# Performance work log

Measured on AMD Instinct MI355X. Metric: run time of the kernel, lower is better.

Reference implementation:

```python
import jax, jax.numpy as jnp
import numpy as np

N_NODES = 50000
N_EDGES = 500000
HIDDEN = 128
HEADS = 8
HEAD_DIM = HIDDEN // HEADS


def setup_inputs() -> dict:
    key = jax.random.key(0)
    ks = jax.random.split(key, 20)

    def lin_w(k, fin, fout):
        return (jax.random.normal(k, (fin, fout), jnp.float32) / np.sqrt(fin)).astype(jnp.float32)

    inp = {
        "h": jax.random.normal(ks[0], (N_NODES, HIDDEN), jnp.float32),
        "x": jax.random.normal(ks[1], (N_NODES, 3), jnp.float32),
        "src": jax.random.randint(ks[2], (N_EDGES,), 0, N_NODES, jnp.int32),
        "dst": jax.random.randint(ks[3], (N_EDGES,), 0, N_NODES, jnp.int32),
        "distances": jax.random.uniform(ks[4], (N_EDGES,), jnp.float32),
        # linear layers stored as [in, out] (transposed vs torch nn.Linear)
        "Wq": lin_w(ks[5], HIDDEN, HIDDEN), "bq": jnp.zeros((HIDDEN,), jnp.float32),
        "Wk": lin_w(ks[6], HIDDEN, HIDDEN), "bk": jnp.zeros((HIDDEN,), jnp.float32),
        "Wv": lin_w(ks[7], HIDDEN, HIDDEN), "bv": jnp.zeros((HIDDEN,), jnp.float32),
        "Wo": lin_w(ks[8], HIDDEN, HIDDEN), "bo": jnp.zeros((HIDDEN,), jnp.float32),
        "Wd": lin_w(ks[9], 1, HEADS), "bd": jnp.zeros((HEADS,), jnp.float32),
        "Wg1": lin_w(ks[10], HIDDEN, HIDDEN), "bg1": jnp.zeros((HIDDEN,), jnp.float32),
        "Wg2": lin_w(ks[11], HIDDEN, 1), "bg2": jnp.zeros((1,), jnp.float32),
    }
    return inp


def reference(h, x, src, dst, distances,
              Wq, bq, Wk, bk, Wv, bv, Wo, bo, Wd, bd, Wg1, bg1, Wg2, bg2):
    n = h.shape[0]
    heads = Wd.shape[1]
    dh = Wq.shape[1] // heads

    q = (h @ Wq + bq).reshape(n, heads, dh)
    k = (h @ Wk + bk).reshape(n, heads, dh)
    v = (h @ Wv + bv).reshape(n, heads, dh)

    q_src = q[src]            # [E, heads, dh]
    k_dst = k[dst]
    v_dst = v[dst]

    logits = jnp.einsum('ehd,ehd->eh', q_src, k_dst) / jnp.sqrt(jnp.asarray(dh, h.dtype))
    bias = (distances * distances)[:, None] @ Wd + bd      # [E, heads]
    lg = logits - bias

    # segment softmax over edges grouped by src node
    m = jax.ops.segment_max(lg, src, num_segments=n)        # [N, heads]
    ex = jnp.exp(lg - m[src])
    s = jax.ops.segment_sum(ex, src, num_segments=n)
    w = ex / jnp.maximum(s[src], 1e-9)                      # [E, heads]

    h_upd = jax.ops.segment_sum(v_dst * w[:, :, None], src, num_segments=n)
    h_out = h + h_upd.reshape(n, heads * dh) @ Wo + bo

    w_mean = w.mean(axis=1)                                 # mean over heads -> [E]
    disp = jax.ops.segment_sum((x[dst] - x[src]) * w_mean[:, None], src, num_segments=n)

    gate = jnp.tanh(jax.nn.silu(h_out @ Wg1 + bg1) @ Wg2 + bg2)  # [N, 1]
    x_out = x + gate * disp
    return (h_out, x_out)
```

## Files before the change

### kernel.cpp

```cpp
#include <hip/hip_runtime.h>
#include <math.h>

#define N_NODES 50000
#define N_EDGES 500000
#define HIDDEN 128
#define HEADS 8
#define HEAD_DIM 16

#define QKV_BLOCKS 1563
#define SCAT_BLOCKS 1954
#define SPLITW_BLOCKS 320
#define ZERO_BLOCKS 196

typedef __attribute__((ext_vector_type(8))) short short8;
typedef __attribute__((ext_vector_type(4))) float floatx4;

#define OFF_Q       0u
#define OFF_KV      6400000u
#define OFF_HHI     12800000u
#define OFF_HLO     16000000u
#define OFF_DISP    19200000u
#define OFF_CNT     19350016u
#define OFF_ROWPTR  19400032u
#define OFF_CURSOR  19450048u
#define OFF_ESD     19500064u
#define OFF_WSPLIT  20500064u

static __device__ __forceinline__ unsigned short f2bf(float f) {
    unsigned u = __builtin_bit_cast(unsigned, f);
    unsigned r = (u + 0x7FFFu + ((u >> 16) & 1u)) >> 16;
    return (unsigned short)r;
}
static __device__ __forceinline__ float bf2f(unsigned short s) {
    return __builtin_bit_cast(float, (unsigned)s << 16);
}

__global__ void k_prep(const float* __restrict__ Wq, const float* __restrict__ Wk,
                       const float* __restrict__ Wv, const float* __restrict__ Wo,
                       const float* __restrict__ Wg1, unsigned short* __restrict__ ws,
                       int* __restrict__ cnt) {
    if (blockIdx.x >= SPLITW_BLOCKS) {
        int i = (blockIdx.x - SPLITW_BLOCKS) * 256 + threadIdx.x;
        if (i < N_NODES) cnt[i] = 0;
        return;
    }
    int t = blockIdx.x * 256 + threadIdx.x;
    int m = t >> 14, r = t & 16383;
    int k = r >> 7, n = r & 127;
    const float* W = (m == 0) ? Wq : (m == 1) ? Wk : (m == 2) ? Wv : (m == 3) ? Wo : Wg1;
    float x = W[k * 128 + n];
    int kc = k >> 5, kin = k & 31, quad = kin >> 3, j = kin & 7;
    int ct = n >> 4, nin = n & 15, lane = quad * 16 + nin;
    unsigned base = ((((unsigned)(m * 4 + kc) * 8 + ct) * 2) * 64 + lane) * 8 + j;
    unsigned short a = f2bf(x);
    ws[base] = a;
    ws[base + 512] = f2bf(x - bf2f(a));
}

__global__ void k_count(const int* __restrict__ src, int* __restrict__ cnt) {
    int e = blockIdx.x * 256 + threadIdx.x;
    if (e < N_EDGES) atomicAdd(&cnt[src[e]], 1);
}

__global__ __launch_bounds__(1024) void k_scan1(const int* __restrict__ cnt,
                                                int* __restrict__ loc,
                                                int* __restrict__ bsum, int n) {
    __shared__ int buf[1024];
    int t = threadIdx.x;
    int i = blockIdx.x * 1024 + t;
    int val = (i < n) ? cnt[i] : 0;
    buf[t] = val;
    __syncthreads();
    for (int off = 1; off < 1024; off <<= 1) {
        int a = (t >= off) ? buf[t - off] : 0;
        __syncthreads();
        buf[t] += a;
        __syncthreads();
    }
    if (i < n) loc[i] = buf[t];
    if (t == 1023) bsum[blockIdx.x] = buf[1023];
}

__global__ __launch_bounds__(256) void k_scan23(const int* __restrict__ cnt,
                                                const int* __restrict__ loc,
                                                const int* __restrict__ bsum,
                                                int* __restrict__ rowptr,
                                                int* __restrict__ cursor, int n, int nb) {
    __shared__ int sb[64];
    int t = threadIdx.x;
    if (t < 64) {
        int v = (t < nb) ? bsum[t] : 0;
        for (int off = 1; off < 64; off <<= 1) {
            int a = __shfl_up(v, off);
            if (t >= off) v += a;
        }
        sb[t] = v;
    }
    __syncthreads();
    int i = blockIdx.x * 256 + t;
    if (i < n) {
        int off = (i >= 1024) ? sb[(i >> 10) - 1] : 0;
        int incl = loc[i] + off;
        rowptr[i + 1] = incl;
        cursor[i] = incl - cnt[i];
    }
    if (i == 0) rowptr[0] = 0;
}

__global__ __launch_bounds__(256) void k_qkv_scatter(
    const float* __restrict__ h, const unsigned short* __restrict__ wsp,
    const float* __restrict__ bq, const float* __restrict__ bk, const float* __restrict__ bv,
    float* __restrict__ q, unsigned* __restrict__ kvp,
    const int* __restrict__ src, const int* __restrict__ dst,
    const float* __restrict__ dist, int* __restrict__ cursor, int2* __restrict__ esd) {
    if (blockIdx.x >= QKV_BLOCKS) {
        int e = (blockIdx.x - QKV_BLOCKS) * 256 + threadIdx.x;
        if (e < N_EDGES) {
            int pos = atomicAdd(&cursor[src[e]], 1);
            float dd = dist[e];
            esd[pos] = make_int2(dst[e], __float_as_int(dd * dd));
        }
        return;
    }

    const int wave = threadIdx.x >> 6, lane = threadIdx.x & 63;
    const int quad = lane >> 4, l15 = lane & 15;
    const int ct0 = wave * 2;
    const int row0 = blockIdx.x * 32;

    floatx4 acc[3][2][2];
#pragma unroll
    for (int m = 0; m < 3; ++m)
#pragma unroll
        for (int c = 0; c < 2; ++c)
#pragma unroll
            for (int r = 0; r < 2; ++r) acc[m][c][r] = (floatx4){0.f, 0.f, 0.f, 0.f};

#pragma unroll
    for (int kc = 0; kc < 4; ++kc) {
        short8 ah[2], al[2];
#pragma unroll
        for (int rt = 0; rt < 2; ++rt) {
            int row = row0 + rt * 16 + l15;
            if (row >= N_NODES) row = N_NODES - 1;
            const float* hp = h + (size_t)row * 128 + kc * 32 + quad * 8;
            float4 f0 = *(const float4*)(hp);
            float4 f1 = *(const float4*)(hp + 4);
            float fv[8] = {f0.x, f0.y, f0.z, f0.w, f1.x, f1.y, f1.z, f1.w};
#pragma unroll
            for (int j = 0; j < 8; ++j) {
                unsigned short hi = f2bf(fv[j]);
                ah[rt][j] = (short)hi;
                al[rt][j] = (short)f2bf(fv[j] - bf2f(hi));
            }
        }
#pragma unroll
        for (int m = 0; m < 3; ++m) {
#pragma unroll
            for (int ctl = 0; ctl < 2; ++ctl) {
                unsigned fb = ((((unsigned)(m * 4 + kc) * 8 + (ct0 + ctl)) * 2) * 64 + lane) * 8;
                short8 bh = *(const short8*)(wsp + fb);
                short8 bl = *(const short8*)(wsp + fb + 512);
#pragma unroll
                for (int rt = 0; rt < 2; ++rt) {
                    acc[m][ctl][rt] = __builtin_amdgcn_mfma_f32_16x16x32_bf16(
                        ah[rt], bh, acc[m][ctl][rt], 0, 0, 0);
                    acc[m][ctl][rt] = __builtin_amdgcn_mfma_f32_16x16x32_bf16(
                        ah[rt], bl, acc[m][ctl][rt], 0, 0, 0);
                    acc[m][ctl][rt] = __builtin_amdgcn_mfma_f32_16x16x32_bf16(
                        al[rt], bh, acc[m][ctl][rt], 0, 0, 0);
                }
            }
        }
    }

#pragma unroll
    for (int ctl = 0; ctl < 2; ++ctl) {
        int col = (ct0 + ctl) * 16 + l15;
        float bq_ = bq[col], bk_ = bk[col], bv_ = bv[col];
#pragma unroll
        for (int rt = 0; rt < 2; ++rt) {
#pragma unroll
            for (int reg = 0; reg < 4; ++reg) {
                int row = row0 + rt * 16 + quad * 4 + reg;
                if (row < N_NODES) {
                    q[(size_t)row * 128 + col] = acc[0][ctl][rt][reg] + bq_;
                    unsigned kb = f2bf(acc[1][ctl][rt][reg] + bk_);
                    unsigned vb = f2bf(acc[2][ctl][rt][reg] + bv_);
                    kvp[(size_t)row * 128 + col] = kb | (vb << 16);
                }
            }
        }
    }
}

__global__ __launch_bounds__(256) void k_edge_node(
    const float* __restrict__ q, const unsigned* __restrict__ kvp,
    const float* __restrict__ x,
    const int2* __restrict__ esd, const int* __restrict__ rowptr,
    const float* __restrict__ Wd, const float* __restrict__ bd,
    unsigned short* __restrict__ hupd_hi, unsigned short* __restrict__ hupd_lo,
    float* __restrict__ disp) {
    const int wave = threadIdx.x >> 6, lane = threadIdx.x & 63;
    const int node = blockIdx.x * 4 + wave;
    const int h = lane >> 3, sub = lane & 7;
    const int beg = rowptr[node], end = rowptr[node + 1];

    const float2 qv = *(const float2*)(q + (size_t)node * 128 + 2 * lane);
    const float wdh = Wd[h], bdh = bd[h];
    const bool dal = (sub < 3);
    float xs = dal ? x[node * 3 + sub] : 0.f;
    const unsigned colo = 2 * lane;

    float acc0 = 0.f, acc1 = 0.f, s_own = 0.f, da = 0.f;

    for (int cb = beg; cb < end; cb += 64) {
        int idx = cb + lane;
        int dvec = 0; float d2vec = 0.f;
        if (idx < end) {
            int2 ed = esd[idx];
            dvec = ed.x;
            d2vec = __int_as_float(ed.y);
        }
        int clen = min(64, end - cb);
        int i = 0;
        for (; i + 4 <= clen; i += 4) {
            int di[4]; float dd2[4]; uint2 kv2[4]; float xg[4];
#pragma unroll
            for (int j = 0; j < 4; ++j) {
                di[j]  = __shfl(dvec, i + j);
                dd2[j] = __shfl(d2vec, i + j);
            }
#pragma unroll
            for (int j = 0; j < 4; ++j)
                kv2[j] = *(const uint2*)(kvp + (unsigned)di[j] * 128u + colo);
#pragma unroll
            for (int j = 0; j < 4; ++j)
                xg[j] = dal ? x[(unsigned)di[j] * 3u + sub] : 0.f;
#pragma unroll
            for (int j = 0; j < 4; ++j) {
                float k0 = __builtin_bit_cast(float, kv2[j].x << 16);
                float v0 = __builtin_bit_cast(float, kv2[j].x & 0xFFFF0000u);
                float k1 = __builtin_bit_cast(float, kv2[j].y << 16);
                float v1 = __builtin_bit_cast(float, kv2[j].y & 0xFFFF0000u);
                float p = qv.x * k0 + qv.y * k1;
                p += __shfl_xor(p, 1);
                p += __shfl_xor(p, 2);
                p += __shfl_xor(p, 4);
                float w = __expf(p * 0.25f - (dd2[j] * wdh + bdh));
                s_own += w;
                acc0 += v0 * w;
                acc1 += v1 * w;
                da += (xg[j] - xs) * w;
            }
        }
        for (; i < clen; ++i) {
            int dij  = __shfl(dvec, i);
            float d2 = __shfl(d2vec, i);
            uint2 kv2 = *(const uint2*)(kvp + (unsigned)dij * 128u + colo);
            float xgj = dal ? x[(unsigned)dij * 3u + sub] : 0.f;
            float k0 = __builtin_bit_cast(float, kv2.x << 16);
            float v0 = __builtin_bit_cast(float, kv2.x & 0xFFFF0000u);
            float k1 = __builtin_bit_cast(float, kv2.y << 16);
            float v1 = __builtin_bit_cast(float, kv2.y & 0xFFFF0000u);
            float p = qv.x * k0 + qv.y * k1;
            p += __shfl_xor(p, 1);
            p += __shfl_xor(p, 2);
            p += __shfl_xor(p, 4);
            float w = __expf(p * 0.25f - (d2 * wdh + bdh));
            s_own += w;
            acc0 += v0 * w;
            acc1 += v1 * w;
            da += (xgj - xs) * w;
        }
    }

    float inva = 1.f / fmaxf(s_own, 1e-9f);
    float o0 = acc0 * inva, o1 = acc1 * inva;
    unsigned short h0 = f2bf(o0), h1 = f2bf(o1);
    unsigned short l0 = f2bf(o0 - bf2f(h0)), l1 = f2bf(o1 - bf2f(h1));
    ((unsigned*)hupd_hi)[(size_t)node * 64 + lane] = (unsigned)h0 | ((unsigned)h1 << 16);
    ((unsigned*)hupd_lo)[(size_t)node * 64 + lane] = (unsigned)l0 | ((unsigned)l1 << 16);

    da *= 0.125f * inva;
    da += __shfl_xor(da, 8);
    da += __shfl_xor(da, 16);
    da += __shfl_xor(da, 32);
    if (lane < 3) disp[node * 3 + lane] = da;
}

__global__ __launch_bounds__(256) void k_hout_gate(
    const float* __restrict__ h,
    const unsigned short* __restrict__ hupd_hi, const unsigned short* __restrict__ hupd_lo,
    const unsigned short* __restrict__ wsp,
    const float* __restrict__ bo, const float* __restrict__ bg1,
    const float* __restrict__ Wg2, const float* __restrict__ bg2,
    const float* __restrict__ x, const float* __restrict__ disp,
    float* __restrict__ hout, float* __restrict__ xout) {
    __shared__ float hb[4][16 * 132];
    const int wave = threadIdx.x >> 6, lane = threadIdx.x & 63;
    const int quad = lane >> 4, l15 = lane & 15;
    const int row0 = blockIdx.x * 64 + wave * 16;
    float* hbw = hb[wave];

    floatx4 acc[8];
#pragma unroll
    for (int c = 0; c < 8; ++c) acc[c] = (floatx4){0.f, 0.f, 0.f, 0.f};
#pragma unroll
    for (int kc = 0; kc < 4; ++kc) {
        int row = row0 + l15;
        if (row >= N_NODES) row = N_NODES - 1;
        size_t aoff = (size_t)row * 128 + kc * 32 + quad * 8;
        short8 ah = *(const short8*)(hupd_hi + aoff);
        short8 al = *(const short8*)(hupd_lo + aoff);
#pragma unroll
        for (int ct = 0; ct < 8; ++ct) {
            unsigned fb = ((((unsigned)(3 * 4 + kc) * 8 + ct) * 2) * 64 + lane) * 8;
            short8 bh = *(const short8*)(wsp + fb);
            short8 bl = *(const short8*)(wsp + fb + 512);
            acc[ct] = __builtin_amdgcn_mfma_f32_16x16x32_bf16(ah, bh, acc[ct], 0, 0, 0);
            acc[ct] = __builtin_amdgcn_mfma_f32_16x16x32_bf16(ah, bl, acc[ct], 0, 0, 0);
            acc[ct] = __builtin_amdgcn_mfma_f32_16x16x32_bf16(al, bh, acc[ct], 0, 0, 0);
        }
    }

#pragma unroll
    for (int ct = 0; ct < 8; ++ct) {
        int col = ct * 16 + l15;
        float bias = bo[col];
#pragma unroll
        for (int reg = 0; reg < 4; ++reg) {
            int row = row0 + quad * 4 + reg;
            float val = acc[ct][reg] + bias;
            if (row < N_NODES) {
                val += h[(size_t)row * 128 + col];
                hout[(size_t)row * 128 + col] = val;
            }
            hbw[(quad * 4 + reg) * 132 + col] = val;
        }
    }
    __asm__ volatile("s_waitcnt lgkmcnt(0)" ::: "memory");

    floatx4 acc2[8];
#pragma unroll
    for (int c = 0; c < 8; ++c) acc2[c] = (floatx4){0.f, 0.f, 0.f, 0.f};
#pragma unroll
    for (int kc = 0; kc < 4; ++kc) {
        const float* ap = hbw + l15 * 132 + kc * 32 + quad * 8;
        float4 f0 = *(const float4*)(ap);
        float4 f1 = *(const float4*)(ap + 4);
        float fv[8] = {f0.x, f0.y, f0.z, f0.w, f1.x, f1.y, f1.z, f1.w};
        short8 ah, al;
#pragma unroll
        for (int j = 0; j < 8; ++j) {
            unsigned short hi = f2bf(fv[j]);
            ah[j] = (short)hi;
            al[j] = (short)f2bf(fv[j] - bf2f(hi));
        }
#pragma unroll
        for (int ct = 0; ct < 8; ++ct) {
            unsigned fb = ((((unsigned)(4 * 4 + kc) * 8 + ct) * 2) * 64 + lane) * 8;
            short8 bh = *(const short8*)(wsp + fb);
            short8 bl = *(const short8*)(wsp + fb + 512);
            acc2[ct] = __builtin_amdgcn_mfma_f32_16x16x32_bf16(ah, bh, acc2[ct], 0, 0, 0);
            acc2[ct] = __builtin_amdgcn_mfma_f32_16x16x32_bf16(ah, bl, acc2[ct], 0, 0, 0);
            acc2[ct] = __builtin_amdgcn_mfma_f32_16x16x32_bf16(al, bh, acc2[ct], 0, 0, 0);
        }
    }

    float pr[4] = {0.f, 0.f, 0.f, 0.f};
#pragma unroll
    for (int ct = 0; ct < 8; ++ct) {
        int col = ct * 16 + l15;
        float b1 = bg1[col];
        float w2 = Wg2[col];
#pragma unroll
        for (int reg = 0; reg < 4; ++reg) {
            float z = acc2[ct][reg] + b1;
            pr[reg] += (z / (1.f + __expf(-z))) * w2;
        }
    }
#pragma unroll
    for (int off = 1; off < 16; off <<= 1) {
#pragma unroll
        for (int reg = 0; reg < 4; ++reg) pr[reg] += __shfl_xor(pr[reg], off);
    }
    if (l15 == 0) {
        float b2 = bg2[0];
#pragma unroll
        for (int reg = 0; reg < 4; ++reg) {
            int row = row0 + quad * 4 + reg;
            if (row < N_NODES) {
                float g = tanhf(pr[reg] + b2);
#pragma unroll
                for (int dd = 0; dd < 3; ++dd) {
                    int oo = row * 3 + dd;
                    xout[oo] = x[oo] + g * disp[oo];
                }
            }
        }
    }
}

extern "C" void kernel_launch(void* const* d_in, const int* in_sizes, int n_in,
                              void* d_out, int out_size, void* d_ws, size_t ws_size,
                              hipStream_t stream) {
    const float* h    = (const float*)d_in[0];
    const float* x    = (const float*)d_in[1];
    const int*   src  = (const int*)d_in[2];
    const int*   dst  = (const int*)d_in[3];
    const float* dist = (const float*)d_in[4];
    const float* Wq = (const float*)d_in[5];  const float* bq = (const float*)d_in[6];
    const float* Wk = (const float*)d_in[7];  const float* bk = (const float*)d_in[8];
    const float* Wv = (const float*)d_in[9];  const float* bv = (const float*)d_in[10];
    const float* Wo = (const float*)d_in[11]; const float* bo = (const float*)d_in[12];
    const float* Wd = (const float*)d_in[13]; const float* bd = (const float*)d_in[14];
    const float* Wg1 = (const float*)d_in[15]; const float* bg1 = (const float*)d_in[16];
    const float* Wg2 = (const float*)d_in[17]; const float* bg2 = (const float*)d_in[18];

    float* ws    = (float*)d_ws;
    float* q     = ws + OFF_Q;
    unsigned* kvp = (unsigned*)(ws + OFF_KV);
    float* disp  = ws + OFF_DISP;
    int* cnt     = (int*)(ws + OFF_CNT);
    int* rowptr  = (int*)(ws + OFF_ROWPTR);
    int* cursor  = (int*)(ws + OFF_CURSOR);
    int2* esd    = (int2*)(ws + OFF_ESD);
    unsigned short* wsp = (unsigned short*)(ws + OFF_WSPLIT);
    int* loc    = (int*)(ws + OFF_Q);
    int* bsum   = (int*)(ws + OFF_Q + 500000u);
    unsigned short* hupd_hi = (unsigned short*)(ws + OFF_HHI);
    unsigned short* hupd_lo = (unsigned short*)(ws + OFF_HLO);
    float* hout = (float*)d_out;
    float* xout = hout + (size_t)N_NODES * HIDDEN;

    const int nscan = (N_NODES + 1023) / 1024;

    k_prep<<<SPLITW_BLOCKS + ZERO_BLOCKS, 256, 0, stream>>>(Wq, Wk, Wv, Wo, Wg1, wsp, cnt);
    k_count<<<SCAT_BLOCKS, 256, 0, stream>>>(src, cnt);
    k_scan1<<<nscan, 1024, 0, stream>>>(cnt, loc, bsum, N_NODES);
    k_scan23<<<ZERO_BLOCKS, 256, 0, stream>>>(cnt, loc, bsum, rowptr, cursor, N_NODES, nscan);
    k_qkv_scatter<<<QKV_BLOCKS + SCAT_BLOCKS, 256, 0, stream>>>(
        h, wsp, bq, bk, bv, q, kvp, src, dst, dist, cursor, esd);
    k_edge_node<<<N_NODES / 4, 256, 0, stream>>>(q, kvp, x, esd, rowptr,
                                                 Wd, bd, hupd_hi, hupd_lo, disp);
    k_hout_gate<<<(N_NODES + 63) / 64, 256, 0, stream>>>(h, hupd_hi, hupd_lo, wsp,
                                                         bo, bg1, Wg2, bg2,
                                                         x, disp, hout, xout);
}
```

Baseline: 269.5 us.

## Stage QKV weight splits in LDS and precompute edge ranks to drop scatter atomics

The QKV projection now gives each block 128 rows. It splits the work into Q blocks and fused K/V blocks, and each of those stages a 64KB hi/lo bf16 weight matrix into LDS, where every wave reuses it across all 8 column tiles. Before, each wave read its weight fragments straight from global memory. The edge scatter also changes: the count kernel records each edge's rank within its source node, so the scatter computes positions from rowptr plus rank instead of doing a second atomic on a cursor array. The costs are a large LDS footprint, which limits occupancy, and an extra rank array stored in the h_upd scratch region. There are also fewer, heavier blocks, and the K/V blocks run two serial stage phases.

After: 259.8 us. 3.6% less time.

```diff
diff --git a/kernel.cpp b/kernel.cpp
--- a/kernel.cpp
+++ b/kernel.cpp
@@ -7,7 +7,8 @@
 #define HEADS 8
 #define HEAD_DIM 16
 
-#define QKV_BLOCKS 1563
+#define QB 391
+#define QKV_TOTAL 782
 #define SCAT_BLOCKS 1954
 #define SPLITW_BLOCKS 320
 #define ZERO_BLOCKS 196
@@ -40,7 +41,7 @@
                        const float* __restrict__ Wg1, unsigned short* __restrict__ ws,
                        int* __restrict__ cnt) {
     if (blockIdx.x >= SPLITW_BLOCKS) {
-        int i = (blockIdx.x - SPLITW_BLOCKS) * 256 + threadIdx.x;
+        int i = (int)(blockIdx.x - SPLITW_BLOCKS) * 256 + threadIdx.x;
         if (i < N_NODES) cnt[i] = 0;
         return;
     }
@@ -57,9 +58,10 @@
     ws[base + 512] = f2bf(x - bf2f(a));
 }
 
-__global__ void k_count(const int* __restrict__ src, int* __restrict__ cnt) {
+__global__ void k_count(const int* __restrict__ src, int* __restrict__ cnt,
+                        int* __restrict__ rnk) {
     int e = blockIdx.x * 256 + threadIdx.x;
-    if (e < N_EDGES) atomicAdd(&cnt[src[e]], 1);
+    if (e < N_EDGES) rnk[e] = atomicAdd(&cnt[src[e]], 1);
 }
 
 __global__ __launch_bounds__(1024) void k_scan1(const int* __restrict__ cnt,
@@ -81,11 +83,9 @@
     if (t == 1023) bsum[blockIdx.x] = buf[1023];
 }
 
-__global__ __launch_bounds__(256) void k_scan23(const int* __restrict__ cnt,
-                                                const int* __restrict__ loc,
+__global__ __launch_bounds__(256) void k_scan23(const int* __restrict__ loc,
                                                 const int* __restrict__ bsum,
-                                                int* __restrict__ rowptr,
-                                                int* __restrict__ cursor, int n, int nb) {
+                                                int* __restrict__ rowptr, int n, int nb) {
     __shared__ int sb[64];
     int t = threadIdx.x;
     if (t < 64) {
@@ -100,96 +100,149 @@
     int i = blockIdx.x * 256 + t;
     if (i < n) {
         int off = (i >= 1024) ? sb[(i >> 10) - 1] : 0;
-        int incl = loc[i] + off;
-        rowptr[i + 1] = incl;
-        cursor[i] = incl - cnt[i];
+        rowptr[i + 1] = loc[i] + off;
     }
     if (i == 0) rowptr[0] = 0;
 }
 
-__global__ __launch_bounds__(256) void k_qkv_scatter(
+__global__ __launch_bounds__(256, 2) void k_qkv_scatter(
     const float* __restrict__ h, const unsigned short* __restrict__ wsp,
     const float* __restrict__ bq, const float* __restrict__ bk, const float* __restrict__ bv,
     float* __restrict__ q, unsigned* __restrict__ kvp,
     const int* __restrict__ src, const int* __restrict__ dst,
-    const float* __restrict__ dist, int* __restrict__ cursor, int2* __restrict__ esd) {
-    if (blockIdx.x >= QKV_BLOCKS) {
-        int e = (blockIdx.x - QKV_BLOCKS) * 256 + threadIdx.x;
+    const float* __restrict__ dist, const int* __restrict__ rowptr,
+    const int* __restrict__ rnk, int2* __restrict__ esd) {
+    if (blockIdx.x >= QKV_TOTAL) {
+        int e = (int)(blockIdx.x - QKV_TOTAL) * 256 + threadIdx.x;
         if (e < N_EDGES) {
-            int pos = atomicAdd(&cursor[src[e]], 1);
+            int s = src[e];
             float dd = dist[e];
+            int pos = rowptr[s] + rnk[e];
             esd[pos] = make_int2(dst[e], __float_as_int(dd * dd));
         }
         return;
     }
 
-    const int wave = threadIdx.x >> 6, lane = threadIdx.x & 63;
+    __shared__ short lds[32768];
+    const int tid = threadIdx.x;
+    const int wave = tid >> 6, lane = tid & 63;
     const int quad = lane >> 4, l15 = lane & 15;
-    const int ct0 = wave * 2;
-    const int row0 = blockIdx.x * 32;
-
-    floatx4 acc[3][2][2];
-#pragma unroll
-    for (int m = 0; m < 3; ++m)
-#pragma unroll
-        for (int c = 0; c < 2; ++c)
-#pragma unroll
-            for (int r = 0; r < 2; ++r) acc[m][c][r] = (floatx4){0.f, 0.f, 0.f, 0.f};
-
-#pragma unroll
-    for (int kc = 0; kc < 4; ++kc) {
-        short8 ah[2], al[2];
-#pragma unroll
-        for (int rt = 0; rt < 2; ++rt) {
-            int row = row0 + rt * 16 + l15;
-            if (row >= N_NODES) row = N_NODES - 1;
-            const float* hp = h + (size_t)row * 128 + kc * 32 + quad * 8;
-            float4 f0 = *(const float4*)(hp);
-            float4 f1 = *(const float4*)(hp + 4);
+    const bool iskv = (blockIdx.x >= QB);
+    const int blk = iskv ? (int)blockIdx.x - QB : (int)blockIdx.x;
+    const int row0 = blk * 128 + wave * 32;
+
+    short8 ah[2][4], al[2][4];
+#pragma unroll
+    for (int rt = 0; rt < 2; ++rt) {
+        int row = row0 + rt * 16 + l15;
+        if (row >= N_NODES) row = N_NODES - 1;
+        const float* hp = h + (size_t)row * 128;
+#pragma unroll
+        for (int kc = 0; kc < 4; ++kc) {
+            const float* p = hp + kc * 32 + quad * 8;
+            float4 f0 = *(const float4*)(p);
+            float4 f1 = *(const float4*)(p + 4);
             float fv[8] = {f0.x, f0.y, f0.z, f0.w, f1.x, f1.y, f1.z, f1.w};
 #pragma unroll
             for (int j = 0; j < 8; ++j) {
                 unsigned short hi = f2bf(fv[j]);
-                ah[rt][j] = (short)hi;
-                al[rt][j] = (short)f2bf(fv[j] - bf2f(hi));
-            }
-        }
-#pragma unroll
-        for (int m = 0; m < 3; ++m) {
-#pragma unroll
-            for (int ctl = 0; ctl < 2; ++ctl) {
-                unsigned fb = ((((unsigned)(m * 4 + kc) * 8 + (ct0 + ctl)) * 2) * 64 + lane) * 8;
-                short8 bh = *(const short8*)(wsp + fb);
-                short8 bl = *(const short8*)(wsp + fb + 512);
+                ah[rt][kc][j] = (short)hi;
+                al[rt][kc][j] = (short)f2bf(fv[j] - bf2f(hi));
+            }
+        }
+    }
+
+    auto stage = [&](int m) {
+        const float4* s4 = (const float4*)(wsp + (unsigned)m * 32768u);
+        float4* d4 = (float4*)lds;
+#pragma unroll 4
+        for (int it = tid; it < 4096; it += 256) d4[it] = s4[it];
+    };
+
+    auto compute = [&](floatx4 (&acc)[2][8]) {
+#pragma unroll
+        for (int kc = 0; kc < 4; ++kc) {
+#pragma unroll
+            for (int ct = 0; ct < 8; ++ct) {
+                const short* tb = lds + (((kc * 8 + ct) * 2) * 64 + lane) * 8;
+                short8 bh = *(const short8*)(tb);
+                short8 bl = *(const short8*)(tb + 512);
 #pragma unroll
                 for (int rt = 0; rt < 2; ++rt) {
-                    acc[m][ctl][rt] = __builtin_amdgcn_mfma_f32_16x16x32_bf16(
-                        ah[rt], bh, acc[m][ctl][rt], 0, 0, 0);
-                    acc[m][ctl][rt] = __builtin_amdgcn_mfma_f32_16x16x32_bf16(
-                        ah[rt], bl, acc[m][ctl][rt], 0, 0, 0);
-                    acc[m][ctl][rt] = __builtin_amdgcn_mfma_f32_16x16x32_bf16(
-                        al[rt], bh, acc[m][ctl][rt], 0, 0, 0);
+                    acc[rt][ct] = __builtin_amdgcn_mfma_f32_16x16x32_bf16(
+                        ah[rt][kc], bh, acc[rt][ct], 0, 0, 0);
+                    acc[rt][ct] = __builtin_amdgcn_mfma_f32_16x16x32_bf16(
+                        ah[rt][kc], bl, acc[rt][ct], 0, 0, 0);
+                    acc[rt][ct] = __builtin_amdgcn_mfma_f32_16x16x32_bf16(
+                        al[rt][kc], bh, acc[rt][ct], 0, 0, 0);
                 }
             }
         }
-    }
-
-#pragma unroll
-    for (int ctl = 0; ctl < 2; ++ctl) {
-        int col = (ct0 + ctl) * 16 + l15;
-        float bq_ = bq[col], bk_ = bk[col], bv_ = bv[col];
-#pragma unroll
-        for (int rt = 0; rt < 2; ++rt) {
-#pragma unroll
-            for (int reg = 0; reg < 4; ++reg) {
-                int row = row0 + rt * 16 + quad * 4 + reg;
-                if (row < N_NODES) {
-                    q[(size_t)row * 128 + col] = acc[0][ctl][rt][reg] + bq_;
-                    unsigned kb = f2bf(acc[1][ctl][rt][reg] + bk_);
-                    unsigned vb = f2bf(acc[2][ctl][rt][reg] + bv_);
-                    kvp[(size_t)row * 128 + col] = kb | (vb << 16);
+    };
+
+    if (!iskv) {
+        stage(0);
+        __syncthreads();
+        floatx4 acc[2][8];
+#pragma unroll
+        for (int rt = 0; rt < 2; ++rt)
+#pragma unroll
+            for (int ct = 0; ct < 8; ++ct) acc[rt][ct] = (floatx4){0.f, 0.f, 0.f, 0.f};
+        compute(acc);
+#pragma unroll
+        for (int ct = 0; ct < 8; ++ct) {
+            int col = ct * 16 + l15;
+            float b = bq[col];
+#pragma unroll
+            for (int rt = 0; rt < 2; ++rt)
+#pragma unroll
+                for (int reg = 0; reg < 4; ++reg) {
+                    int row = row0 + rt * 16 + quad * 4 + reg;
+                    if (row < N_NODES) q[(size_t)row * 128 + col] = acc[rt][ct][reg] + b;
                 }
-            }
+        }
+    } else {
+        stage(1);
+        __syncthreads();
+        floatx4 acc[2][8];
+#pragma unroll
+        for (int rt = 0; rt < 2; ++rt)
+#pragma unroll
+            for (int ct = 0; ct < 8; ++ct) acc[rt][ct] = (floatx4){0.f, 0.f, 0.f, 0.f};
+        compute(acc);
+        unsigned kb[2][8][2];
+#pragma unroll
+        for (int ct = 0; ct < 8; ++ct) {
+            float b = bk[ct * 16 + l15];
+#pragma unroll
+            for (int rt = 0; rt < 2; ++rt) {
+                kb[rt][ct][0] = (unsigned)f2bf(acc[rt][ct][0] + b) |
+                                ((unsigned)f2bf(acc[rt][ct][1] + b) << 16);
+                kb[rt][ct][1] = (unsigned)f2bf(acc[rt][ct][2] + b) |
+                                ((unsigned)f2bf(acc[rt][ct][3] + b) << 16);
+            }
+        }
+        __syncthreads();
+        stage(2);
+        __syncthreads();
+#pragma unroll
+        for (int rt = 0; rt < 2; ++rt)
+#pragma unroll
+            for (int ct = 0; ct < 8; ++ct) acc[rt][ct] = (floatx4){0.f, 0.f, 0.f, 0.f};
+        compute(acc);
+#pragma unroll
+        for (int ct = 0; ct < 8; ++ct) {
+            int col = ct * 16 + l15;
+            float b = bv[col];
+#pragma unroll
+            for (int rt = 0; rt < 2; ++rt)
+#pragma unroll
+                for (int reg = 0; reg < 4; ++reg) {
+                    int row = row0 + rt * 16 + quad * 4 + reg;
+                    unsigned vb = f2bf(acc[rt][ct][reg] + b);
+                    unsigned kw = (kb[rt][ct][reg >> 1] >> ((reg & 1) * 16)) & 0xFFFFu;
+                    if (row < N_NODES) kvp[(size_t)row * 128 + col] = kw | (vb << 16);
+                }
         }
     }
 }
@@ -424,11 +477,11 @@
     float* disp  = ws + OFF_DISP;
     int* cnt     = (int*)(ws + OFF_CNT);
     int* rowptr  = (int*)(ws + OFF_ROWPTR);
-    int* cursor  = (int*)(ws + OFF_CURSOR);
     int2* esd    = (int2*)(ws + OFF_ESD);
     unsigned short* wsp = (unsigned short*)(ws + OFF_WSPLIT);
     int* loc    = (int*)(ws + OFF_Q);
     int* bsum   = (int*)(ws + OFF_Q + 500000u);
+    int* rank   = (int*)(ws + OFF_HHI);
     unsigned short* hupd_hi = (unsigned short*)(ws + OFF_HHI);
     unsigned short* hupd_lo = (unsigned short*)(ws + OFF_HLO);
     float* hout = (float*)d_out;
@@ -437,11 +490,11 @@
     const int nscan = (N_NODES + 1023) / 1024;
 
     k_prep<<<SPLITW_BLOCKS + ZERO_BLOCKS, 256, 0, stream>>>(Wq, Wk, Wv, Wo, Wg1, wsp, cnt);
-    k_count<<<SCAT_BLOCKS, 256, 0, stream>>>(src, cnt);
+    k_count<<<SCAT_BLOCKS, 256, 0, stream>>>(src, cnt, rank);
     k_scan1<<<nscan, 1024, 0, stream>>>(cnt, loc, bsum, N_NODES);
-    k_scan23<<<ZERO_BLOCKS, 256, 0, stream>>>(cnt, loc, bsum, rowptr, cursor, N_NODES, nscan);
-    k_qkv_scatter<<<QKV_BLOCKS + SCAT_BLOCKS, 256, 0, stream>>>(
-        h, wsp, bq, bk, bv, q, kvp, src, dst, dist, cursor, esd);
+    k_scan23<<<ZERO_BLOCKS, 256, 0, stream>>>(loc, bsum, rowptr, N_NODES, nscan);
+    k_qkv_scatter<<<QKV_TOTAL + SCAT_BLOCKS, 256, 0, stream>>>(
+        h, wsp, bq, bk, bv, q, kvp, src, dst, dist, rowptr, rank, esd);
     k_edge_node<<<N_NODES / 4, 256, 0, stream>>>(q, kvp, x, esd, rowptr,
                                                  Wd, bd, hupd_hi, hupd_lo, disp);
     k_hout_gate<<<(N_NODES + 63) / 64, 256, 0, stream>>>(h, hupd_hi, hupd_lo, wsp,
```
